# Kernel tuning notes

Measured on AMD Instinct MI355X. Metric: run time of the kernel, lower is better.

Reference implementation:

```python
import jax, jax.numpy as jnp
import numpy as np

IMG = 640
SCORE_THR = 0.1
IOU_THR = 0.5
MAX_DET = 200  # fixed upper bound on kept boxes per class (jit-static)
BBOX_STD = (0.1, 0.1, 0.2, 0.2)  # standard RetinaNet delta std


def _make_anchors():
    # Standard RetinaNet anchors: P3-P7, 3 ratios x 3 scales, xyxy format.
    strides = [8, 16, 32, 64, 128]
    sizes = [32, 64, 128, 256, 512]
    ratios = np.array([0.5, 1.0, 2.0])
    scales = np.array([2 ** 0, 2 ** (1.0 / 3.0), 2 ** (2.0 / 3.0)])
    out = []
    for stride, size in zip(strides, sizes):
        n = IMG // stride
        ws = (size * scales[None, :] * np.sqrt(1.0 / ratios)[:, None]).reshape(-1)
        hs = (size * scales[None, :] * np.sqrt(ratios)[:, None]).reshape(-1)
        c = (np.arange(n) + 0.5) * stride
        CX, CY = np.meshgrid(c, c)
        ctr = np.stack([CX.ravel(), CY.ravel()], -1)  # [n*n, 2]
        wh = np.stack([ws, hs], -1)  # [9, 2]
        boxes = np.concatenate([ctr[:, None, :] - 0.5 * wh[None],
                                ctr[:, None, :] + 0.5 * wh[None]], -1)  # [n*n, 9, 4]
        out.append(boxes.reshape(-1, 4))
    return np.concatenate(out, 0).astype(np.float32)  # [76725, 4]


def setup_inputs() -> dict:
    key = jax.random.key(0)
    k1, k2 = jax.random.split(key)
    A = 76725
    C = 80
    classification = jax.random.uniform(k1, (1, A, C), dtype=jnp.float32)
    regression = jax.random.normal(k2, (1, A, 4), dtype=jnp.float32)
    anchors = jnp.asarray(_make_anchors())  # [A, 4] xyxy
    return {"classification": classification, "regression": regression, "anchors": anchors}


def _decode_and_clip(anchors, reg):
    aw = anchors[:, 2] - anchors[:, 0]
    ah = anchors[:, 3] - anchors[:, 1]
    ax = anchors[:, 0] + 0.5 * aw
    ay = anchors[:, 1] + 0.5 * ah
    cx = ax + reg[:, 0] * BBOX_STD[0] * aw
    cy = ay + reg[:, 1] * BBOX_STD[1] * ah
    w = aw * jnp.exp(reg[:, 2] * BBOX_STD[2])
    h = ah * jnp.exp(reg[:, 3] * BBOX_STD[3])
    x1 = jnp.clip(cx - 0.5 * w, 0.0, IMG)  # trimBox2Image
    y1 = jnp.clip(cy - 0.5 * h, 0.0, IMG)
    x2 = jnp.clip(cx + 0.5 * w, 0.0, IMG)
    y2 = jnp.clip(cy + 0.5 * h, 0.0, IMG)
    return jnp.stack([x1, y1, x2, y2], -1)  # [A, 4]


def reference(classification, regression, anchors):
    cls = classification[0]  # [A, C]
    boxes = _decode_and_clip(anchors, regression[0])  # [A, 4]
    A = cls.shape[0]
    C = cls.shape[1]
    idx = jnp.arange(A)
    areas = (boxes[:, 2] - boxes[:, 0]) * (boxes[:, 3] - boxes[:, 1])

    def nms_one(scores):  # scores: [A] for one class
        s0 = jnp.where(scores > SCORE_THR, scores, -1.0)
        keep0 = jnp.zeros((A,), dtype=bool)

        def step(carry, _):
            s, keep = carry
            i = jnp.argmax(s)
            valid = s[i] > 0.0
            keep = keep.at[i].set(valid)
            b = boxes[i]
            ix1 = jnp.maximum(b[0], boxes[:, 0])
            iy1 = jnp.maximum(b[1], boxes[:, 1])
            ix2 = jnp.minimum(b[2], boxes[:, 2])
            iy2 = jnp.minimum(b[3], boxes[:, 3])
            inter = jnp.clip(ix2 - ix1, 0.0) * jnp.clip(iy2 - iy1, 0.0)
            ab = (b[2] - b[0]) * (b[3] - b[1])
            iou = inter / (ab + areas - inter)
            sup = valid & ((iou > IOU_THR) | (idx == i))
            s = jnp.where(sup, -1.0, s)
            return (s, keep), None

        (_, keep), _ = jax.lax.scan(step, (s0, keep0), None, length=MAX_DET)
        return keep

    keep = jax.vmap(nms_one)(cls.T)  # [C, A] bool, greedy NMS per class
    final_scores = jnp.where(keep, cls.T, 0.0)  # [C, A]
    final_labels = jnp.where(keep, jnp.arange(C, dtype=jnp.int32)[:, None], -1)  # [C, A]
    final_boxes = jnp.where(keep[..., None], boxes[None], 0.0)  # [C, A, 4]
    return final_scores, final_labels, final_boxes, keep
```

## Files before the change

### kernel.cpp

```cpp
#include <hip/hip_runtime.h>
#include <cstdint>
#include <cstddef>

#pragma clang fp contract(off)

#define A_N 76725
#define C_N 80
#define CA_N (A_N * 80)
#define MAXDET 200
#define NBIN 16
#define BCAP 256
#define W_N 320
#define WORDS 5
#define IMG_F 640.0f
#define THR0 0.975f
#define CNT_STRIDE 32
#define FILLB 2480

typedef unsigned long long u64;

__device__ __forceinline__ bool iou_gt(float b0, float b1, float b2, float b3, float ab,
                                       float x0, float x1, float x2, float x3, float xa) {
    float ix1 = fmaxf(b0, x0);
    float iy1 = fmaxf(b1, x1);
    float ix2 = fminf(b2, x2);
    float iy2 = fminf(b3, x3);
    float iw = fmaxf(ix2 - ix1, 0.0f);
    float ih = fmaxf(iy2 - iy1, 0.0f);
    float inter = iw * ih;
    float den = ab + xa - inter;
    float iou = inter / den;
    return iou > 0.5f;
}

__device__ __forceinline__ float band_lo(int b) {
    return 0.975f - 0.025f * (float)b;
}

__device__ __forceinline__ u64 readlane64(u64 v, int src) {
    unsigned lo = __builtin_amdgcn_readlane((unsigned)v, src);
    unsigned hi = __builtin_amdgcn_readlane((unsigned)(v >> 32), src);
    return ((u64)hi << 32) | lo;
}

__global__ __launch_bounds__(256) void k_prep(const float* __restrict__ cls,
                                              const float* __restrict__ reg,
                                              const float* __restrict__ anc,
                                              float* __restrict__ boxes,
                                              int* __restrict__ gcnt,
                                              u64* __restrict__ gkeys) {
    int i = blockIdx.x * 256 + threadIdx.x;
    if (i < A_N) {
        float a0 = anc[i * 4 + 0], a1 = anc[i * 4 + 1];
        float a2 = anc[i * 4 + 2], a3 = anc[i * 4 + 3];
        float aw = a2 - a0;
        float ah = a3 - a1;
        float ax = a0 + 0.5f * aw;
        float ay = a1 + 0.5f * ah;
        float r0 = reg[i * 4 + 0], r1 = reg[i * 4 + 1];
        float r2 = reg[i * 4 + 2], r3 = reg[i * 4 + 3];
        float cx = ax + r0 * 0.1f * aw;
        float cy = ay + r1 * 0.1f * ah;
        float w = aw * expf(r2 * 0.2f);
        float h = ah * expf(r3 * 0.2f);
        float x1 = fminf(fmaxf(cx - 0.5f * w, 0.0f), IMG_F);
        float y1 = fminf(fmaxf(cy - 0.5f * h, 0.0f), IMG_F);
        float x2 = fminf(fmaxf(cx + 0.5f * w, 0.0f), IMG_F);
        float y2 = fminf(fmaxf(cy + 0.5f * h, 0.0f), IMG_F);
        boxes[i * 4 + 0] = x1;
        boxes[i * 4 + 1] = y1;
        boxes[i * 4 + 2] = x2;
        boxes[i * 4 + 3] = y2;
    }
    if (i < CA_N) {
        float s = cls[i];
        if (s > THR0) {
            int c = i % C_N;
            unsigned a = (unsigned)(i / C_N);
            int b = (int)((s - THR0) * 640.0f);
            b = b < 0 ? 0 : (b > (NBIN - 1) ? (NBIN - 1) : b);
            int slot = atomicAdd(&gcnt[(c * NBIN + b) * CNT_STRIDE], 1);
            if (slot < BCAP)
                gkeys[((size_t)(c * NBIN + b) << 8) + slot] =
                    ((u64)__float_as_uint(s) << 32) | (u64)(0xFFFFFFFFu - a);
        }
    }
}

__device__ __forceinline__ int resolve_run(const u64* seg, int cnt, int kept,
                                           const float4* __restrict__ boxes4,
                                           float4* kboxS, float* karea,
                                           int* kIdxL, float* kScrL,
                                           float4* cbxS, float* car64,
                                           unsigned int* mlo, unsigned int* mhi,
                                           unsigned char* supp, int* keptL,
                                           int tid, int lane) {
    for (int cs = 0; cs < cnt && kept < MAXDET; cs += 64) {
        int nc = (cnt - cs < 64) ? (cnt - cs) : 64;
        float4 rb = make_float4(0.f, 0.f, 0.f, 0.f);
        float rar = 0.f, rsc = 0.f;
        int rix = 0;
        if (tid < 64) {
            mlo[tid] = 0;
            mhi[tid] = 0;
            supp[tid] = (tid < nc) ? 0 : 1;
            if (tid < nc) {
                u64 key = seg[cs + tid];
                rix = (int)(0xFFFFFFFFu - (unsigned)(key & 0xFFFFFFFFull));
                rsc = __uint_as_float((unsigned)(key >> 32));
                rb = boxes4[rix];
                rar = (rb.z - rb.x) * (rb.w - rb.y);
                cbxS[tid] = rb;
                car64[tid] = rar;
            }
        }
        __syncthreads();
        {
            int i = tid >> 4, jl = tid & 15;
            if (i < nc) {
                float4 x = cbxS[i];
                float xa = car64[i];
                bool s = false;
                for (int j = jl; j < kept; j += 16) {
                    float4 kb = kboxS[j];
                    if (iou_gt(kb.x, kb.y, kb.z, kb.w, karea[j],
                               x.x, x.y, x.z, x.w, xa)) { s = true; break; }
                }
                if (s) supp[i] = 1;
            }
        }
        {
            int i = tid & 63, jb2 = tid >> 6;
            if (i < nc) {
                float4 b = cbxS[i];
                float ba = car64[i];
                unsigned int l32 = 0, h32 = 0;
                for (int j = jb2; j < nc; j += 16) {
                    if (j > i) {
                        float4 o = cbxS[j];
                        if (iou_gt(b.x, b.y, b.z, b.w, ba,
                                   o.x, o.y, o.z, o.w, car64[j])) {
                            if (j < 32) l32 |= 1u << j;
                            else        h32 |= 1u << (j - 32);
                        }
                    }
                }
                if (l32) atomicOr(&mlo[i], l32);
                if (h32) atomicOr(&mhi[i], h32);
            }
        }
        __syncthreads();
        if (tid < 64) {
            bool alive = (lane < nc) && (supp[lane] == 0);
            unsigned int myLo = mlo[lane], myHi = mhi[lane];
            int kc = kept;
            while (kc < MAXDET) {
                u64 av = __ballot(alive);
                if (av == 0ull) break;
                int i = (int)__builtin_ctzll(av);
                unsigned int plo = (unsigned)__shfl((int)myLo, i, 64);
                unsigned int phi = (unsigned)__shfl((int)myHi, i, 64);
                u64 mi = ((u64)phi << 32) | plo;
                if (lane == i) {
                    kboxS[kc] = rb;
                    karea[kc] = rar;
                    kIdxL[kc] = rix;
                    kScrL[kc] = rsc;
                    alive = false;
                }
                if ((mi >> lane) & 1ull) alive = false;
                kc++;
            }
            if (lane == 0) *keptL = kc;
        }
        __syncthreads();
        kept = *keptL;
    }
    return kept;
}

__global__ __launch_bounds__(1024) void k_mega(const float* __restrict__ cls,
                                               const float* __restrict__ boxes,
                                               const int* __restrict__ gcnt,
                                               const u64* __restrict__ gkeys,
                                               int* __restrict__ kcnt,
                                               int* __restrict__ kidx,
                                               float* __restrict__ kscr,
                                               float* __restrict__ kboxg,
                                               float4* __restrict__ out4) {
    const int tid = threadIdx.x;

    if (blockIdx.x >= C_N) {
        int fb = blockIdx.x - C_N;
        const int n4 = (7 * CA_N) / 4;
        const int lab_lo = CA_N / 4;
        const int lab_hi = (2 * CA_N) / 4;
        for (int i = fb * 1024 + tid; i < n4; i += FILLB * 1024) {
            float v = (i >= lab_lo && i < lab_hi) ? -1.0f : 0.0f;
            out4[i] = make_float4(v, v, v, v);
        }
        return;
    }

    const int c = blockIdx.x;
    const int wave = tid >> 6, lane = tid & 63;
    const float4* boxes4 = (const float4*)boxes;

    __shared__ u64 buf[NBIN][BCAP];
    __shared__ u64 maskS[W_N * WORDS];
    __shared__ float4 cbx[W_N];
    __shared__ float car[W_N];
    __shared__ float cscr[W_N];
    __shared__ int cidx[W_N];
    __shared__ float4 kboxS[MAXDET];
    __shared__ float karea[MAXDET];
    __shared__ int kIdxL[MAXDET];
    __shared__ float kScrL[MAXDET];
    __shared__ float4 cbxS[64];
    __shared__ float car64[64];
    __shared__ unsigned int mlo[64], mhi[64];
    __shared__ unsigned char supp[64];
    __shared__ int cntb[NBIN], off[NBIN];
    __shared__ u64 kmS[WORDS];
    __shared__ int keptShv, keptCtr, cntL, keptL;

    if (tid < NBIN) {
        int v = gcnt[(c * NBIN + tid) * CNT_STRIDE];
        cntb[tid] = v > BCAP ? BCAP : v;
    }
    if (tid == 0) keptCtr = 0;
    __syncthreads();
    if (tid < NBIN) {
        int s = 0;
        for (int bb = NBIN - 1; bb > tid; --bb) s += cntb[bb];
        off[tid] = s;
    }
    __syncthreads();
    const int N = off[0] + cntb[0];
    const int NW = N < W_N ? N : W_N;

    {
        int cw = cntb[wave];
        volatile u64* seg = buf[wave];
        const u64* src = gkeys + ((size_t)(c * NBIN + wave) << 8);
        for (int i = lane; i < cw; i += 64) seg[i] = src[i];
        int n2 = 64;
        while (n2 < cw) n2 <<= 1;
        for (int i = cw + lane; i < n2; i += 64) seg[i] = 0ull;
        __builtin_amdgcn_wave_barrier();
        for (int k = 2; k <= n2; k <<= 1) {
            for (int j = k >> 1; j > 0; j >>= 1) {
                for (int i0 = lane; i0 < n2; i0 += 64) {
                    int ixj = i0 ^ j;
                    if (ixj > i0) {
                        u64 u = seg[i0], v = seg[ixj];
                        bool up = ((i0 & k) == 0);
                        if (up ? (u < v) : (u > v)) { seg[i0] = v; seg[ixj] = u; }
                    }
                }
                __builtin_amdgcn_wave_barrier();
            }
        }
    }
    __syncthreads();

    for (int i = tid; i < NW; i += 1024) {
        int b = NBIN - 1;
        for (; b >= 0; --b)
            if (i >= off[b] && i < off[b] + cntb[b]) break;
        u64 key = buf[b][i - off[b]];
        int a = (int)(0xFFFFFFFFu - (unsigned)(key & 0xFFFFFFFFull));
        float4 bx = boxes4[a];
        cbx[i] = bx;
        car[i] = (bx.z - bx.x) * (bx.w - bx.y);
        cscr[i] = __uint_as_float((unsigned)(key >> 32));
        cidx[i] = a;
    }
    __syncthreads();

    for (int idx = tid; idx < W_N * WORDS; idx += 1024) {
        int r = idx / WORDS, w = idx - r * WORDS;
        u64 m = 0;
        if (r < NW) {
            int jbase = w * 64;
            int jend = (NW - jbase) < 64 ? (NW - jbase) : 64;
            if (jend > 0 && jbase + 63 > r) {
                float4 rb = cbx[r];
                float ra = car[r];
                for (int jj = 0; jj < jend; ++jj) {
                    int jg = jbase + jj;
                    if (jg > r) {
                        float4 o = cbx[jg];
                        if (iou_gt(rb.x, rb.y, rb.z, rb.w, ra,
                                   o.x, o.y, o.z, o.w, car[jg]))
                            m |= 1ull << jj;
                    }
                }
            }
        }
        maskS[idx] = m;
    }
    __syncthreads();

    if (tid < 64) {
        int kept = 0;
        u64 rem0 = 0, rem1 = 0, rem2 = 0, rem3 = 0, rem4 = 0;
        u64 km0 = 0, km1 = 0, km2 = 0, km3 = 0, km4 = 0;

#define SCAN_CHUNK(W0)                                                        \
        if (W0 * 64 < NW && kept < MAXDET) {                                  \
            int r = W0 * 64 + lane;                                           \
            u64 r0 = maskS[r * WORDS + 0];                                    \
            u64 r1 = maskS[r * WORDS + 1];                                    \
            u64 r2 = maskS[r * WORDS + 2];                                    \
            u64 r3 = maskS[r * WORDS + 3];                                    \
            u64 r4 = maskS[r * WORDS + 4];                                    \
            int nb = NW - W0 * 64;                                            \
            u64 valw = nb >= 64 ? ~0ull : ((1ull << nb) - 1ull);              \
            u64 alive = ~rem##W0 & valw;                                      \
            while (alive && kept < MAXDET) {                                  \
                int ii = (int)__builtin_ctzll(alive);                         \
                u64 q0 = readlane64(r0, ii);                                  \
                u64 q1 = readlane64(r1, ii);                                  \
                u64 q2 = readlane64(r2, ii);                                  \
                u64 q3 = readlane64(r3, ii);                                  \
                u64 q4 = readlane64(r4, ii);                                  \
                rem0 |= q0; rem1 |= q1; rem2 |= q2; rem3 |= q3; rem4 |= q4;   \
                km##W0 |= 1ull << ii;                                         \
                kept++;                                                       \
                alive &= ~(q##W0 | (1ull << ii));                             \
            }                                                                 \
        }

        SCAN_CHUNK(0)
        SCAN_CHUNK(1)
        SCAN_CHUNK(2)
        SCAN_CHUNK(3)
        SCAN_CHUNK(4)
#undef SCAN_CHUNK

        if (lane == 0) {
            kmS[0] = km0; kmS[1] = km1; kmS[2] = km2; kmS[3] = km3; kmS[4] = km4;
            keptShv = kept;
        }
    }
    __syncthreads();

    for (int i = tid; i < NW; i += 1024) {
        if ((kmS[i >> 6] >> (i & 63)) & 1ull) {
            int slot = atomicAdd(&keptCtr, 1);
            kboxS[slot] = cbx[i];
            karea[slot] = car[i];
            kIdxL[slot] = cidx[i];
            kScrL[slot] = cscr[i];
        }
    }
    __syncthreads();
    int kept = keptShv;

    if (kept < MAXDET && N > NW) {
        for (int b = NBIN - 1; b >= 0 && kept < MAXDET; --b) {
            int s0 = off[b], sz = cntb[b];
            int start = NW > s0 ? (NW - s0) : 0;
            if (start < sz)
                kept = resolve_run((const u64*)buf[b] + start, sz - start, kept,
                                   boxes4, kboxS, karea, kIdxL, kScrL,
                                   cbxS, car64, mlo, mhi, supp, &keptL,
                                   tid, lane);
        }
    }

    if (kept < MAXDET) {
        u64* keysF = &buf[0][0];
        for (int band = 1;; ++band) {
            float hiB = band_lo(band - 1);
            float lo = band_lo(band);
            bool last = (lo <= 0.1f);
            float loEff = last ? 0.1f : lo;
            if (tid == 0) cntL = 0;
            __syncthreads();
            for (int a = tid; a < A_N; a += 1024) {
                float s = cls[(size_t)a * C_N + c];
                if (s > loEff && s <= hiB) {
                    int p = atomicAdd(&cntL, 1);
                    if (p < 4096)
                        keysF[p] = ((u64)__float_as_uint(s) << 32) |
                                   (u64)(0xFFFFFFFFu - (unsigned)a);
                }
            }
            __syncthreads();
            int cnt = cntL < 4096 ? cntL : 4096;
            int n2 = 64;
            while (n2 < cnt) n2 <<= 1;
            for (int i = cnt + tid; i < n2; i += 1024) keysF[i] = 0ull;
            __syncthreads();
            for (int k = 2; k <= n2; k <<= 1) {
                for (int j = k >> 1; j > 0; j >>= 1) {
                    for (int i = tid; i < n2; i += 1024) {
                        int ixj = i ^ j;
                        if (ixj > i) {
                            u64 u = keysF[i], v = keysF[ixj];
                            bool up = ((i & k) == 0);
                            if (up ? (u < v) : (u > v)) { keysF[i] = v; keysF[ixj] = u; }
                        }
                    }
                    __syncthreads();
                }
            }
            kept = resolve_run(keysF, cnt, kept, boxes4,
                               kboxS, karea, kIdxL, kScrL,
                               cbxS, car64, mlo, mhi, supp, &keptL, tid, lane);
            if (kept >= MAXDET || last) break;
        }
    }

    if (tid == 0) kcnt[c] = kept;
    for (int i = tid; i < kept; i += 1024) {
        kidx[c * MAXDET + i] = kIdxL[i];
        kscr[c * MAXDET + i] = kScrL[i];
        float4 kb = kboxS[i];
        kboxg[(c * MAXDET + i) * 4 + 0] = kb.x;
        kboxg[(c * MAXDET + i) * 4 + 1] = kb.y;
        kboxg[(c * MAXDET + i) * 4 + 2] = kb.z;
        kboxg[(c * MAXDET + i) * 4 + 3] = kb.w;
    }
}

__global__ __launch_bounds__(256) void k_scatter(const int* __restrict__ kcnt,
                                                 const int* __restrict__ kidx,
                                                 const float* __restrict__ kscr,
                                                 const float* __restrict__ kboxg,
                                                 float* __restrict__ out) {
    int c = blockIdx.x, t = threadIdx.x;
    int k = kcnt[c];
    for (int i = t; i < k; i += 256) {
        int a = kidx[c * MAXDET + i];
        size_t base = (size_t)c * A_N + (size_t)a;
        out[base] = kscr[c * MAXDET + i];
        out[(size_t)CA_N + base] = (float)c;
        size_t bo = (size_t)2 * CA_N + base * 4;
        out[bo + 0] = kboxg[(c * MAXDET + i) * 4 + 0];
        out[bo + 1] = kboxg[(c * MAXDET + i) * 4 + 1];
        out[bo + 2] = kboxg[(c * MAXDET + i) * 4 + 2];
        out[bo + 3] = kboxg[(c * MAXDET + i) * 4 + 3];
        out[(size_t)6 * CA_N + base] = 1.0f;
    }
}

extern "C" void kernel_launch(void* const* d_in, const int* in_sizes, int n_in,
                              void* d_out, int out_size, void* d_ws, size_t ws_size,
                              hipStream_t stream) {
    const float* cls = (const float*)d_in[0];
    const float* reg = (const float*)d_in[1];
    const float* anc = (const float*)d_in[2];
    float* out = (float*)d_out;

    int* gcnt = (int*)d_ws;
    float* boxes = (float*)(gcnt + C_N * NBIN * CNT_STRIDE);
    u64* gkeys = (u64*)(boxes + 4 * A_N);
    int* kcnt = (int*)(gkeys + (size_t)C_N * NBIN * BCAP);
    int* kidx = kcnt + C_N;
    float* kscr = (float*)(kidx + C_N * MAXDET);
    float* kboxg = kscr + C_N * MAXDET;

    hipMemsetAsync(gcnt, 0, C_N * NBIN * CNT_STRIDE * sizeof(int), stream);

    k_prep<<<(CA_N + 255) / 256, 256, 0, stream>>>(cls, reg, anc, boxes, gcnt, gkeys);

    k_mega<<<C_N + FILLB, 1024, 0, stream>>>(cls, boxes, gcnt, gkeys,
                                             kcnt, kidx, kscr, kboxg, (float4*)d_out);

    k_scatter<<<C_N, 256, 0, stream>>>(kcnt, kidx, kscr, kboxg, out);
}
```

Baseline: 270.6 us.

## Replace per-bin bitonic sort with rank sort and batch NMS mask propagation

Each bin's per-wave bitonic sort of up to 256 keys in shared memory is replaced by a rank (counting) sort. Each lane counts how many keys beat its own keys, then scatters them into place. This removes the log² barrier stages. The greedy NMS scan now reads only the diagonal mask word per chunk in its serial loop, then propagates suppression to later chunks with one OR-reduction across kept lanes per word. This cuts the readlane work per kept box. The rank sort costs O(n) LDS reads per lane and assumes distinct keys; equal keys would collide on the same slot.

```diff
diff --git a/kernel.cpp b/kernel.cpp
--- a/kernel.cpp
+++ b/kernel.cpp
@@ -41,6 +41,15 @@
     unsigned lo = __builtin_amdgcn_readlane((unsigned)v, src);
     unsigned hi = __builtin_amdgcn_readlane((unsigned)(v >> 32), src);
     return ((u64)hi << 32) | lo;
+}
+
+__device__ __forceinline__ u64 or_reduce64(u64 v) {
+    for (int m = 1; m < 64; m <<= 1) {
+        unsigned lo = (unsigned)__shfl_xor((int)(unsigned)v, m, 64);
+        unsigned hi = (unsigned)__shfl_xor((int)(unsigned)(v >> 32), m, 64);
+        v |= ((u64)hi << 32) | lo;
+    }
+    return v;
 }
 
 __global__ __launch_bounds__(256) void k_prep(const float* __restrict__ cls,
@@ -241,26 +250,31 @@
 
     {
         int cw = cntb[wave];
-        volatile u64* seg = buf[wave];
+        u64* seg = buf[wave];
         const u64* src = gkeys + ((size_t)(c * NBIN + wave) << 8);
-        for (int i = lane; i < cw; i += 64) seg[i] = src[i];
-        int n2 = 64;
-        while (n2 < cw) n2 <<= 1;
-        for (int i = cw + lane; i < n2; i += 64) seg[i] = 0ull;
+        u64 myk[4];
+        int myi[4], myn = 0;
+        for (int i = lane; i < cw; i += 64) {
+            u64 k = src[i];
+            seg[i] = k;
+            myk[myn] = k;
+            myi[myn] = i;
+            ++myn;
+        }
+        int rk0 = 0, rk1 = 0, rk2 = 0, rk3 = 0;
+        for (int j = 0; j < cw; ++j) {
+            u64 kj = seg[j];
+            if (myn > 0) rk0 += (kj > myk[0]);
+            if (myn > 1) rk1 += (kj > myk[1]);
+            if (myn > 2) rk2 += (kj > myk[2]);
+            if (myn > 3) rk3 += (kj > myk[3]);
+        }
+        (void)myi;
         __builtin_amdgcn_wave_barrier();
-        for (int k = 2; k <= n2; k <<= 1) {
-            for (int j = k >> 1; j > 0; j >>= 1) {
-                for (int i0 = lane; i0 < n2; i0 += 64) {
-                    int ixj = i0 ^ j;
-                    if (ixj > i0) {
-                        u64 u = seg[i0], v = seg[ixj];
-                        bool up = ((i0 & k) == 0);
-                        if (up ? (u < v) : (u > v)) { seg[i0] = v; seg[ixj] = u; }
-                    }
-                }
-                __builtin_amdgcn_wave_barrier();
-            }
-        }
+        if (myn > 0) seg[rk0] = myk[0];
+        if (myn > 1) seg[rk1] = myk[1];
+        if (myn > 2) seg[rk2] = myk[2];
+        if (myn > 3) seg[rk3] = myk[3];
     }
     __syncthreads();
 
@@ -304,45 +318,42 @@
 
     if (tid < 64) {
         int kept = 0;
-        u64 rem0 = 0, rem1 = 0, rem2 = 0, rem3 = 0, rem4 = 0;
-        u64 km0 = 0, km1 = 0, km2 = 0, km3 = 0, km4 = 0;
-
-#define SCAN_CHUNK(W0)                                                        \
-        if (W0 * 64 < NW && kept < MAXDET) {                                  \
-            int r = W0 * 64 + lane;                                           \
-            u64 r0 = maskS[r * WORDS + 0];                                    \
-            u64 r1 = maskS[r * WORDS + 1];                                    \
-            u64 r2 = maskS[r * WORDS + 2];                                    \
-            u64 r3 = maskS[r * WORDS + 3];                                    \
-            u64 r4 = maskS[r * WORDS + 4];                                    \
-            int nb = NW - W0 * 64;                                            \
-            u64 valw = nb >= 64 ? ~0ull : ((1ull << nb) - 1ull);              \
-            u64 alive = ~rem##W0 & valw;                                      \
-            while (alive && kept < MAXDET) {                                  \
-                int ii = (int)__builtin_ctzll(alive);                         \
-                u64 q0 = readlane64(r0, ii);                                  \
-                u64 q1 = readlane64(r1, ii);                                  \
-                u64 q2 = readlane64(r2, ii);                                  \
-                u64 q3 = readlane64(r3, ii);                                  \
-                u64 q4 = readlane64(r4, ii);                                  \
-                rem0 |= q0; rem1 |= q1; rem2 |= q2; rem3 |= q3; rem4 |= q4;   \
-                km##W0 |= 1ull << ii;                                         \
-                kept++;                                                       \
-                alive &= ~(q##W0 | (1ull << ii));                             \
-            }                                                                 \
-        }
-
-        SCAN_CHUNK(0)
-        SCAN_CHUNK(1)
-        SCAN_CHUNK(2)
-        SCAN_CHUNK(3)
-        SCAN_CHUNK(4)
-#undef SCAN_CHUNK
-
-        if (lane == 0) {
-            kmS[0] = km0; kmS[1] = km1; kmS[2] = km2; kmS[3] = km3; kmS[4] = km4;
-            keptShv = kept;
-        }
+        u64 rem1 = 0, rem2 = 0, rem3 = 0, rem4 = 0;
+        u64 km[WORDS] = {0, 0, 0, 0, 0};
+
+        for (int W = 0; W < WORDS; ++W) {
+            if (W * 64 >= NW || kept >= MAXDET) break;
+            int row = W * 64 + lane;
+            u64 rdiag = (row < NW) ? maskS[row * WORDS + W] : 0ull;
+            int nb = NW - W * 64;
+            u64 valw = nb >= 64 ? ~0ull : ((1ull << nb) - 1ull);
+            u64 remW = (W == 1) ? rem1 : (W == 2) ? rem2 : (W == 3) ? rem3 :
+                       (W == 4) ? rem4 : 0ull;
+            u64 alive = ~remW & valw;
+            u64 kmW = 0;
+            while (alive && kept < MAXDET) {
+                int ii = (int)__builtin_ctzll(alive);
+                u64 q = readlane64(rdiag, ii);
+                kmW |= 1ull << ii;
+                kept++;
+                alive &= ~(q | (1ull << ii));
+            }
+            km[W] = kmW;
+            if (kept >= MAXDET) break;
+            bool keptlane = (kmW >> lane) & 1ull;
+            for (int w = W + 1; w < WORDS; ++w) {
+                if (w * 64 >= NW) break;
+                u64 rw = (row < NW && keptlane) ? maskS[row * WORDS + w] : 0ull;
+                rw = or_reduce64(rw);
+                u64 contrib = readlane64(rw, 0);
+                if (w == 1) rem1 |= contrib;
+                else if (w == 2) rem2 |= contrib;
+                else if (w == 3) rem3 |= contrib;
+                else rem4 |= contrib;
+            }
+        }
+        if (lane < WORDS) kmS[lane] = km[lane];
+        if (lane == 0) keptShv = kept;
     }
     __syncthreads();
 
```

After: 234.0 us. -13.5%, faster.
